# Kernel optimization log

Measured on AMD Instinct MI355X. Metric: run time of the kernel, lower is better.

## Reference

```python
import jax, jax.numpy as jnp
import numpy as np

QMIN, QMAX = 0.0, 255.0  # uint8 export range

def _round_half_away(x):
    # torch _round_nearest_without_round: round half away from zero
    return jnp.where(x < 0, -jnp.floor(-x + 0.5), jnp.floor(x + 0.5))

def setup_inputs() -> dict:
    key = jax.random.key(0)
    k = jax.random.split(key, 7)
    B, S, DIN, DOUT = 2, 2048, 2048, 8192
    x = jax.random.normal(k[0], (B, S, DIN), dtype=jnp.float32)
    # per-tensor activation qparams (keep scale away from 0)
    a_scale = jax.random.uniform(k[1], (1,), dtype=jnp.float32) * 0.05 + 0.01
    a_zp = jax.random.randint(k[2], (1,), 100, 156, dtype=jnp.int32)
    # pre-quantized uint8 weight stored as int32, per-out-channel qparams
    weight_q = jax.random.randint(k[3], (DOUT, DIN), 0, 256, dtype=jnp.int32)
    w_scale = jax.random.uniform(k[4], (DOUT,), dtype=jnp.float32) * 0.02 + 0.001
    w_zp = jax.random.randint(k[5], (DOUT,), 100, 156, dtype=jnp.int32)
    bias = jax.random.normal(k[6], (DOUT,), dtype=jnp.float32)
    return {"x": x, "a_scale": a_scale, "a_zp": a_zp, "weight_q": weight_q,
            "w_scale": w_scale, "w_zp": w_zp, "bias": bias}

def reference(x, a_scale, a_zp, weight_q, w_scale, w_zp, bias):
    dt = x.dtype
    # --- activation fake-quant (ExportAffineQuantizer, per-tensor) ---
    s = a_scale.astype(dt).reshape((1,) * x.ndim)
    z = a_zp.astype(dt).reshape((1,) * x.ndim)
    x_q = jnp.clip(_round_half_away(x / s) + z, QMIN, QMAX)
    x_dq = (x_q - z) * s
    # --- weight dequant (ExportWeightBackedLinear, ch_axis=0) ---
    # W: [out, in] = (w_q - zp) * scale, broadcast over in-dim
    W = (weight_q.astype(dt) - w_zp.astype(dt)[:, None]) * w_scale.astype(dt)[:, None]
    # --- linear: [B,S,in] @ [in,out] + bias ---
    return jnp.einsum('bsk,ok->bso', x_dq, W) + bias.astype(dt)
```

## Files before the change

### kernel.cpp

```cpp
#include <hip/hip_runtime.h>
#include <hip/hip_bf16.h>

#define M_DIM 4096
#define K_DIM 2048
#define N_DIM 8192

typedef int   int32x4  __attribute__((ext_vector_type(4)));
typedef int   int32x16 __attribute__((ext_vector_type(16)));

#define XC_OFF 0
#define WC_OFF 8388608UL
#define RX_OFF 25165824UL
#define AL_OFF 25182208UL
#define G_OFF  25214976UL
#define F0_OFF 25247744UL

__device__ __forceinline__ int pack4(int a, int b, int c, int d) {
    return (a & 255) | ((b & 255) << 8) | ((c & 255) << 16) | ((d & 255) << 24);
}

__global__ __launch_bounds__(256) void prep_x_kernel(
    const float4* __restrict__ x, signed char* __restrict__ xc, int* __restrict__ rx,
    const float* __restrict__ a_scale, const int* __restrict__ a_zp)
{
    const int row = blockIdx.x;
    const int tid = threadIdx.x;
    const float s = a_scale[0];
    const float z = (float)a_zp[0];
    int sum = 0;
    int* xci = (int*)(xc + (size_t)row * K_DIM);
    const float4* xr = x + (size_t)row * (K_DIM / 4);
    #pragma unroll
    for (int it = 0; it < 2; ++it) {
        int qi = tid + it * 256;
        float4 v = xr[qi];
        int q0 = (int)(fminf(fmaxf(roundf(v.x / s) + z, 0.f), 255.f)) - 128;
        int q1 = (int)(fminf(fmaxf(roundf(v.y / s) + z, 0.f), 255.f)) - 128;
        int q2 = (int)(fminf(fmaxf(roundf(v.z / s) + z, 0.f), 255.f)) - 128;
        int q3 = (int)(fminf(fmaxf(roundf(v.w / s) + z, 0.f), 255.f)) - 128;
        sum += q0 + q1 + q2 + q3;
        xci[qi] = pack4(q0, q1, q2, q3);
    }
    #pragma unroll
    for (int off = 32; off > 0; off >>= 1) sum += __shfl_down(sum, off);
    __shared__ int wsum[4];
    if ((tid & 63) == 0) wsum[tid >> 6] = sum;
    __syncthreads();
    if (tid == 0) rx[row] = wsum[0] + wsum[1] + wsum[2] + wsum[3];
}

__global__ __launch_bounds__(256) void prep_w_kernel(
    const int4* __restrict__ wq, signed char* __restrict__ wc,
    int* __restrict__ al, float* __restrict__ g, float* __restrict__ F0,
    const float* __restrict__ a_scale, const int* __restrict__ a_zp,
    const float* __restrict__ w_scale, const int* __restrict__ w_zp,
    const float* __restrict__ bias)
{
    const int o   = blockIdx.x;
    const int tid = threadIdx.x;
    int sum = 0;
    int* wci = (int*)(wc + (size_t)o * K_DIM);
    const int4* wr = wq + (size_t)o * (K_DIM / 4);
    #pragma unroll
    for (int it = 0; it < 2; ++it) {
        int qi = tid + it * 256;
        int4 v = wr[qi];
        int q0 = v.x - 128, q1 = v.y - 128, q2 = v.z - 128, q3 = v.w - 128;
        sum += q0 + q1 + q2 + q3;
        wci[qi] = pack4(q0, q1, q2, q3);
    }
    #pragma unroll
    for (int off = 32; off > 0; off >>= 1) sum += __shfl_down(sum, off);
    __shared__ int wsum[4];
    if ((tid & 63) == 0) wsum[tid >> 6] = sum;
    __syncthreads();
    if (tid == 0) {
        int rw    = wsum[0] + wsum[1] + wsum[2] + wsum[3];
        int alpha = 128 - w_zp[o];
        int beta  = 128 - a_zp[0];
        int C0    = beta * (rw + K_DIM * alpha);
        float gg  = a_scale[0] * w_scale[o];
        al[o] = alpha;
        g[o]  = gg;
        F0[o] = gg * (float)C0 + bias[o];
    }
}


__device__ __forceinline__ void glds16(const void* gptr, void* lptr) {
    __builtin_amdgcn_global_load_lds(
        (const __attribute__((address_space(1))) void*)gptr,
        (__attribute__((address_space(3))) void*)lptr, 16, 0, 0);
}

__global__ __launch_bounds__(512) void gemm_i8_kernel(
    const signed char* __restrict__ A,
    const signed char* __restrict__ Bw,
    const int*   __restrict__ rx,
    const int*   __restrict__ al,
    const float* __restrict__ g,
    const float* __restrict__ F0,
    float* __restrict__ C)
{
    extern __shared__ signed char lds[];
    signed char* ldsA = lds;
    signed char* ldsB = lds + 65536;

    const int tid  = threadIdx.x;
    const int lane = tid & 63;
    const int wave = tid >> 6;
    const int wr   = wave >> 2;
    const int wc   = wave & 3;
    const int l31  = lane & 31;
    const int lk   = lane >> 5;

    const int bid = blockIdx.x;
    const int swz = (bid & 7) * 64 + (bid >> 3);
    const int bn0 = (swz & 31) * 256;
    const int bm0 = (swz >> 5) * 256;

    const int slr = tid >> 3;
    const int cg  = (tid & 7) ^ (slr & 7);
    const int sp  = cg >> 2;
    const int skc = cg & 3;
    const signed char* srcA0 = A  + (size_t)(bm0 + 2 * slr + sp) * K_DIM + skc * 16;
    const signed char* srcA1 = srcA0 + (size_t)128 * K_DIM;
    const signed char* srcB0 = Bw + (size_t)(bn0 + 2 * slr + sp) * K_DIM + skc * 16;
    const signed char* srcB1 = srcB0 + (size_t)128 * K_DIM;
    signed char* dstA0 = ldsA + tid * 16;
    signed char* dstB0 = ldsB + tid * 16;

#define STAGE_A(s) { const int kof = (s) * 64; const int bo = ((s) & 3) * 16384; \
    glds16(srcA0 + kof, dstA0 + bo); glds16(srcA1 + kof, dstA0 + bo + 8192); }
#define STAGE_B(s) { const int kof = (s) * 64; const int bo = ((s) & 3) * 16384; \
    glds16(srcB0 + kof, dstB0 + bo); glds16(srcB1 + kof, dstB0 + bo + 8192); }

    const int q  = l31 >> 1;
    const int e  = q & 7;
    const int pp = l31 & 1;
    int arowb[4], browb[2];
    #pragma unroll
    for (int im = 0; im < 4; ++im) arowb[im] = (wr * 64 + im * 16 + q) * 128;
    #pragma unroll
    for (int jn = 0; jn < 2; ++jn) browb[jn] = (wc * 32 + jn * 16 + q) * 128;
    const int aoff0 = ((pp * 4 + lk) ^ e) * 16;
    const int aoff1 = aoff0 ^ 32;
    (void)aoff1;

    int32x16 acc[4][2];
    #pragma unroll
    for (int im = 0; im < 4; ++im)
        #pragma unroll
        for (int jn = 0; jn < 2; ++jn)
            acc[im][jn] = (int32x16)(0);

#define TILE_PH(T, AOFF, STAGE_STMT) { \
    const int bo_ = ((T) & 3) * 16384; \
    int32x4 af[4], bf[2]; \
    _Pragma("unroll") for (int im = 0; im < 4; ++im) \
        af[im] = *(const int32x4*)(ldsA + bo_ + arowb[im] + (AOFF)); \
    _Pragma("unroll") for (int jn = 0; jn < 2; ++jn) \
        bf[jn] = *(const int32x4*)(ldsB + bo_ + browb[jn] + (AOFF)); \
    STAGE_STMT; \
    __builtin_amdgcn_s_barrier(); \
    __builtin_amdgcn_s_setprio(1); \
    _Pragma("unroll") for (int im = 0; im < 4; ++im) \
        _Pragma("unroll") for (int jn = 0; jn < 2; ++jn) \
            acc[im][jn] = __builtin_amdgcn_mfma_i32_32x32x32_i8(af[im], bf[jn], acc[im][jn], 0, 0, 0); \
    __builtin_amdgcn_s_setprio(0); \
}

#define BOUND(N) { asm volatile("s_waitcnt vmcnt(" #N ")" ::: "memory"); __builtin_amdgcn_s_barrier(); }

    STAGE_A(0); STAGE_B(0);
    STAGE_A(1); STAGE_B(1);
    STAGE_A(2); STAGE_B(2);
    asm volatile("s_waitcnt vmcnt(8)" ::: "memory");
    __builtin_amdgcn_s_barrier();

    #pragma unroll 1
    for (int t = 0; t < 29; ++t) {
        TILE_PH(t, aoff0, STAGE_A(t + 3));
        TILE_PH(t, aoff1, STAGE_B(t + 3));
        BOUND(8);
    }
    TILE_PH(29, aoff0, ((void)0));
    TILE_PH(29, aoff1, ((void)0)); BOUND(4);
    TILE_PH(30, aoff0, ((void)0));
    TILE_PH(30, aoff1, ((void)0)); BOUND(0);
    TILE_PH(31, aoff0, ((void)0));
    TILE_PH(31, aoff1, ((void)0));

    #pragma unroll
    for (int im = 0; im < 4; ++im) {
        int rxv[16];
        #pragma unroll
        for (int r = 0; r < 16; ++r)
            rxv[r] = rx[bm0 + wr * 128 + im * 32 + (r & 3) + 8 * (r >> 2) + 4 * lk];
        #pragma unroll
        for (int jn = 0; jn < 2; ++jn) {
            const int col = bn0 + wc * 64 + jn * 32 + l31;
            const float gg = g[col];
            const float ff = F0[col];
            const int   aa = al[col];
            #pragma unroll
            for (int r = 0; r < 16; ++r) {
                const int grow = bm0 + wr * 128 + im * 32 + (r & 3) + 8 * (r >> 2) + 4 * lk;
                const int tv = acc[im][jn][r] + aa * rxv[r];
                C[(size_t)grow * N_DIM + col] = fmaf(gg, (float)tv, ff);
            }
        }
    }
#undef TILE_PH
#undef STAGE_A
#undef STAGE_B
#undef BOUND
}


extern "C" void kernel_launch(void* const* d_in, const int* in_sizes, int n_in,
                              void* d_out, int out_size, void* d_ws, size_t ws_size,
                              hipStream_t stream) {
    const float* x        = (const float*)d_in[0];
    const float* a_scale  = (const float*)d_in[1];
    const int*   a_zp     = (const int*)d_in[2];
    const int*   weight_q = (const int*)d_in[3];
    const float* w_scale  = (const float*)d_in[4];
    const int*   w_zp     = (const int*)d_in[5];
    const float* bias     = (const float*)d_in[6];
    float*       out      = (float*)d_out;

    char* ws = (char*)d_ws;
    signed char* xc = (signed char*)(ws + XC_OFF);
    signed char* wc = (signed char*)(ws + WC_OFF);
    int*   rx = (int*)(ws + RX_OFF);
    int*   al = (int*)(ws + AL_OFF);
    float* g  = (float*)(ws + G_OFF);
    float* F0 = (float*)(ws + F0_OFF);

    prep_x_kernel<<<M_DIM, 256, 0, stream>>>((const float4*)x, xc, rx, a_scale, a_zp);
    prep_w_kernel<<<N_DIM, 256, 0, stream>>>((const int4*)weight_q, wc, al, g, F0,
                                             a_scale, a_zp, w_scale, w_zp, bias);

    gemm_i8_kernel<<<512, 512, 131072, stream>>>(xc, wc, rx, al, g, F0, out);
}
```

Measured before the change: 288.9 us.

## Merge per-tile pipeline phases into one barrier and remap block tiling

Each K-tile now loads both halves of the A/B fragments from LDS, waits on outstanding global loads and crosses a single barrier before issuing the next stage's global-to-LDS copies and all 16 MFMAs. Before, each tile had two half-phases, each with its own barrier, plus a separate wait-and-barrier at the end. The block-to-tile mapping also changes from a simple XCD swizzle to a 4x4-style grouped mapping per XCD, meant to improve L2 reuse of A and B panels. The single-barrier schedule holds more fragment registers live, and the wait counts must stay correct for the ring buffer.

Result: no change. 288.6 us (-0.1%).

```diff
diff --git a/kernel.cpp b/kernel.cpp
--- a/kernel.cpp
+++ b/kernel.cpp
@@ -115,9 +115,10 @@
     const int lk   = lane >> 5;
 
     const int bid = blockIdx.x;
-    const int swz = (bid & 7) * 64 + (bid >> 3);
-    const int bn0 = (swz & 31) * 256;
-    const int bm0 = (swz >> 5) * 256;
+    const int x7  = bid & 7;
+    const int lcl = bid >> 3;
+    const int bm0 = ((x7 & 3) * 4 + (lcl & 3)) * 256;
+    const int bn0 = ((x7 >> 2) * 16 + (lcl >> 2)) * 256;
 
     const int slr = tid >> 3;
     const int cg  = (tid & 7) ^ (slr & 7);
@@ -130,9 +131,8 @@
     signed char* dstA0 = ldsA + tid * 16;
     signed char* dstB0 = ldsB + tid * 16;
 
-#define STAGE_A(s) { const int kof = (s) * 64; const int bo = ((s) & 3) * 16384; \
-    glds16(srcA0 + kof, dstA0 + bo); glds16(srcA1 + kof, dstA0 + bo + 8192); }
-#define STAGE_B(s) { const int kof = (s) * 64; const int bo = ((s) & 3) * 16384; \
+#define STAGE(s) { const int kof = (s) * 64; const int bo = ((s) & 3) * 16384; \
+    glds16(srcA0 + kof, dstA0 + bo); glds16(srcA1 + kof, dstA0 + bo + 8192); \
     glds16(srcB0 + kof, dstB0 + bo); glds16(srcB1 + kof, dstB0 + bo + 8192); }
 
     const int q  = l31 >> 1;
@@ -145,7 +145,6 @@
     for (int jn = 0; jn < 2; ++jn) browb[jn] = (wc * 32 + jn * 16 + q) * 128;
     const int aoff0 = ((pp * 4 + lk) ^ e) * 16;
     const int aoff1 = aoff0 ^ 32;
-    (void)aoff1;
 
     int32x16 acc[4][2];
     #pragma unroll
@@ -154,42 +153,42 @@
         for (int jn = 0; jn < 2; ++jn)
             acc[im][jn] = (int32x16)(0);
 
-#define TILE_PH(T, AOFF, STAGE_STMT) { \
+#define TILE(T, VMC, STAGE_STMT) { \
     const int bo_ = ((T) & 3) * 16384; \
-    int32x4 af[4], bf[2]; \
-    _Pragma("unroll") for (int im = 0; im < 4; ++im) \
-        af[im] = *(const int32x4*)(ldsA + bo_ + arowb[im] + (AOFF)); \
+    int32x4 a0[4], b0[2], a1[4], b1[2]; \
+    _Pragma("unroll") for (int im = 0; im < 4; ++im) \
+        a0[im] = *(const int32x4*)(ldsA + bo_ + arowb[im] + aoff0); \
     _Pragma("unroll") for (int jn = 0; jn < 2; ++jn) \
-        bf[jn] = *(const int32x4*)(ldsB + bo_ + browb[jn] + (AOFF)); \
+        b0[jn] = *(const int32x4*)(ldsB + bo_ + browb[jn] + aoff0); \
+    _Pragma("unroll") for (int im = 0; im < 4; ++im) \
+        a1[im] = *(const int32x4*)(ldsA + bo_ + arowb[im] + aoff1); \
+    _Pragma("unroll") for (int jn = 0; jn < 2; ++jn) \
+        b1[jn] = *(const int32x4*)(ldsB + bo_ + browb[jn] + aoff1); \
+    asm volatile("s_waitcnt vmcnt(" #VMC ")" ::: "memory"); \
+    __builtin_amdgcn_s_barrier(); \
+    __builtin_amdgcn_sched_barrier(0); \
     STAGE_STMT; \
-    __builtin_amdgcn_s_barrier(); \
     __builtin_amdgcn_s_setprio(1); \
     _Pragma("unroll") for (int im = 0; im < 4; ++im) \
         _Pragma("unroll") for (int jn = 0; jn < 2; ++jn) \
-            acc[im][jn] = __builtin_amdgcn_mfma_i32_32x32x32_i8(af[im], bf[jn], acc[im][jn], 0, 0, 0); \
+            acc[im][jn] = __builtin_amdgcn_mfma_i32_32x32x32_i8(a0[im], b0[jn], acc[im][jn], 0, 0, 0); \
+    _Pragma("unroll") for (int im = 0; im < 4; ++im) \
+        _Pragma("unroll") for (int jn = 0; jn < 2; ++jn) \
+            acc[im][jn] = __builtin_amdgcn_mfma_i32_32x32x32_i8(a1[im], b1[jn], acc[im][jn], 0, 0, 0); \
     __builtin_amdgcn_s_setprio(0); \
 }
 
-#define BOUND(N) { asm volatile("s_waitcnt vmcnt(" #N ")" ::: "memory"); __builtin_amdgcn_s_barrier(); }
-
-    STAGE_A(0); STAGE_B(0);
-    STAGE_A(1); STAGE_B(1);
-    STAGE_A(2); STAGE_B(2);
+    STAGE(0); STAGE(1); STAGE(2);
     asm volatile("s_waitcnt vmcnt(8)" ::: "memory");
     __builtin_amdgcn_s_barrier();
 
     #pragma unroll 1
     for (int t = 0; t < 29; ++t) {
-        TILE_PH(t, aoff0, STAGE_A(t + 3));
-        TILE_PH(t, aoff1, STAGE_B(t + 3));
-        BOUND(8);
-    }
-    TILE_PH(29, aoff0, ((void)0));
-    TILE_PH(29, aoff1, ((void)0)); BOUND(4);
-    TILE_PH(30, aoff0, ((void)0));
-    TILE_PH(30, aoff1, ((void)0)); BOUND(0);
-    TILE_PH(31, aoff0, ((void)0));
-    TILE_PH(31, aoff1, ((void)0));
+        TILE(t, 4, STAGE(t + 3));
+    }
+    TILE(29, 4, ((void)0));
+    TILE(30, 0, ((void)0));
+    TILE(31, 0, ((void)0));
 
     #pragma unroll
     for (int im = 0; im < 4; ++im) {
@@ -211,10 +210,8 @@
             }
         }
     }
-#undef TILE_PH
-#undef STAGE_A
-#undef STAGE_B
-#undef BOUND
+#undef TILE
+#undef STAGE
 }
 
 
```
